# Kernel tuning notes

Measured on AMD Instinct MI355X. Metric: run time of the kernel, lower is better.

The kernel has to match this reference:

```python
import jax, jax.numpy as jnp
import numpy as np
import math

B, T, D = 4, 4096, 1024
H, M = 16, 64
Dh = D // H


def _rope_tables(head_dim, max_seq_len, base=10000):
    inv_freq = 1.0 / (base ** (np.arange(0, head_dim, 2, dtype=np.float32) / head_dim))
    t = np.arange(max_seq_len, dtype=np.float32)
    freqs = np.einsum('i,j->ij', t, inv_freq)  # [T, Dh/2]
    cos = np.cos(freqs)
    sin = np.sin(freqs)
    # interleave (c, c) pairwise -> [T, Dh]
    cos = np.stack((cos, cos), axis=-1).reshape(max_seq_len, head_dim)
    sin = np.stack((sin, sin), axis=-1).reshape(max_seq_len, head_dim)
    return jnp.asarray(cos), jnp.asarray(sin)


def setup_inputs() -> dict:
    key = jax.random.key(0)
    ks = jax.random.split(key, 6)
    s = 1.0 / math.sqrt(D)
    x = jax.random.normal(ks[0], (B, T, D), dtype=jnp.float32)
    Wq = jnp.clip(jax.random.normal(ks[1], (D, D)) * s, -2 * s, 2 * s).astype(jnp.float32)
    Wk = jnp.clip(jax.random.normal(ks[2], (D, D)) * s, -2 * s, 2 * s).astype(jnp.float32)
    Wv = jnp.clip(jax.random.normal(ks[3], (D, D)) * s, -2 * s, 2 * s).astype(jnp.float32)
    Wo = jnp.clip(jax.random.normal(ks[4], (D, D)) * s, -2 * s, 2 * s).astype(jnp.float32)
    latent_code = (jax.random.normal(ks[5], (H, M, Dh)) * 0.02).astype(jnp.float32)
    rope_cos, rope_sin = _rope_tables(Dh, T)
    mask = jnp.ones((B, 1, T, 1), dtype=jnp.int32)
    return {'x': x, 'Wq': Wq, 'Wk': Wk, 'Wv': Wv, 'Wo': Wo,
            'latent_code': latent_code, 'rope_cos': rope_cos,
            'rope_sin': rope_sin, 'mask': mask}


def _rotate(x):
    # (x1, x2) pairs -> (-x2, x1), interleaved
    x2 = x.reshape(*x.shape[:-1], -1, 2)
    return jnp.stack((-x2[..., 1], x2[..., 0]), axis=-1).reshape(x.shape)


def reference(x, Wq, Wk, Wv, Wo, latent_code, rope_cos, rope_sin, mask):
    Bc, Tc, Dc = x.shape
    scale = 1.0 / math.sqrt(Dh)
    # projections -> [B, H, T, Dh]
    q = (x @ Wq.T).reshape(Bc, Tc, H, Dh).transpose(0, 2, 1, 3)
    k = (x @ Wk.T).reshape(Bc, Tc, H, Dh).transpose(0, 2, 1, 3)
    v = (x @ Wv.T).reshape(Bc, Tc, H, Dh).transpose(0, 2, 1, 3)
    cos = rope_cos[:Tc][None, None]  # [1,1,T,Dh]
    sin = rope_sin[:Tc][None, None]
    q = q * cos + _rotate(q) * sin
    k = k * cos + _rotate(k) * sin
    # Stage 1: token -> latent assignment, softmax over tokens (axis=2)
    assign_logits = jnp.einsum('bhtd,hmd->bhtm', k, latent_code) * scale
    assign_logits = jnp.where(mask == 0, -jnp.inf, assign_logits)
    assign = jax.nn.softmax(assign_logits, axis=2)
    k_lat = jnp.einsum('bhtm,bhtd->bhmd', assign, k)
    v_lat = jnp.einsum('bhtm,bhtd->bhmd', assign, v)
    # Stage 2: query attends to latents, softmax over latents (axis=-1)
    att2 = jnp.einsum('bhtd,bhmd->bhtm', q, k_lat) * scale
    p2 = jax.nn.softmax(att2, axis=-1)
    out = jnp.einsum('bhtm,bhmd->bhtd', p2, v_lat)
    out = out.transpose(0, 2, 1, 3).reshape(Bc, Tc, Dc)
    return out @ Wo.T
```

## Files before the change

kernel.cpp:

```cpp
#include <hip/hip_runtime.h>
#include <hip/hip_bf16.h>
#include <stdint.h>


#define DEV static __device__ __forceinline__

using short8 = __attribute__((ext_vector_type(8))) short;
using f32x4  = __attribute__((ext_vector_type(4))) float;

#define ZERO4 (f32x4){0.f, 0.f, 0.f, 0.f}

DEV float bf2f(unsigned short u) {
  union { unsigned int i; float f; } c; c.i = ((unsigned int)u) << 16; return c.f;
}
DEV unsigned short f2bf(float f) {
  __hip_bfloat16 h = __float2bfloat16(f);
  unsigned short u; __builtin_memcpy(&u, &h, 2); return u;
}
DEV f32x4 mfma16(short8 a, short8 b, f32x4 c) {
  return __builtin_amdgcn_mfma_f32_16x16x32_bf16(a, b, c, 0, 0, 0);
}
#define GLOAD_LDS16(G, L) __builtin_amdgcn_global_load_lds( \
    (const __attribute__((address_space(1))) void*)(G),     \
    (__attribute__((address_space(3))) void*)(L), 16, 0, 0)

__global__ void cvt_all(const float* __restrict__ x,
                        const float* __restrict__ Wq, const float* __restrict__ Wk,
                        const float* __restrict__ Wv, const float* __restrict__ Wo,
                        __hip_bfloat16* __restrict__ xb,
                        __hip_bfloat16* __restrict__ Wb) {
  const int bid = blockIdx.x;
  const float* src;
  __hip_bfloat16* dst;
  int base;
  if (bid < 16384) {
    src = x; dst = xb; base = bid;
  } else {
    const int k = (bid - 16384) >> 10;
    src = (k == 0) ? Wq : (k == 1) ? Wk : (k == 2) ? Wv : Wo;
    dst = Wb + (size_t)k * 1048576;
    base = (bid - 16384) & 1023;
  }
  const int i = (base * 256 + threadIdx.x) * 4;
  const float4 v = *(const float4*)(src + i);
  ushort4 o;
  o.x = f2bf(v.x); o.y = f2bf(v.y); o.z = f2bf(v.z); o.w = f2bf(v.w);
  *(ushort4*)(dst + i) = o;
}

template<int MODE, int ROPE>
__global__ __launch_bounds__(256, 4)
void gemm128b(const __hip_bfloat16* __restrict__ A,
              const __hip_bfloat16* __restrict__ Bt,
              void* __restrict__ Cout, __hip_bfloat16* __restrict__ Ct,
              const float* __restrict__ cosT, const float* __restrict__ sinT,
              int M, int N, int K) {
  __shared__ __hip_bfloat16 As[2][128 * 32];
  __shared__ __hip_bfloat16 Bs[2][128 * 32];
  const int tid = threadIdx.x;
  const int w = tid >> 6, l = tid & 63;
  const int lr = l & 15, lg = l >> 4;
  const int rowA0 = blockIdx.x * 128;
  const int colB0 = blockIdx.y * 128;
  const int srow = w * 16 + (l >> 2);
  const int skk  = (l & 3) * 8;
  const __hip_bfloat16* Ab = A  + (size_t)(rowA0 + srow) * K + skk;
  const __hip_bfloat16* Bb = Bt + (size_t)(colB0 + srow) * K + skk;
  f32x4 acc[4][4];
#pragma unroll
  for (int i = 0; i < 4; ++i)
#pragma unroll
    for (int j = 0; j < 4; ++j) acc[i][j] = ZERO4;
  const int wr = (w >> 1) * 64, wc = (w & 1) * 64;
  const int NT = K >> 5;

#define G_STAGE(kt, buf)                                                   \
  {                                                                        \
    const int k0s = (kt) * 32;                                             \
    GLOAD_LDS16(Ab + k0s,                  &As[buf][(w * 16) * 32]);       \
    GLOAD_LDS16(Ab + (size_t)64 * K + k0s, &As[buf][(64 + w * 16) * 32]);  \
    GLOAD_LDS16(Bb + k0s,                  &Bs[buf][(w * 16) * 32]);       \
    GLOAD_LDS16(Bb + (size_t)64 * K + k0s, &Bs[buf][(64 + w * 16) * 32]);  \
  }

  G_STAGE(0, 0);
  for (int kt = 0; kt < NT; ++kt) {
    const int cur = kt & 1;
    if (kt + 1 < NT) {
      G_STAGE(kt + 1, cur ^ 1);
      asm volatile("s_waitcnt vmcnt(4)" ::: "memory");
    } else {
      asm volatile("s_waitcnt vmcnt(0)" ::: "memory");
    }
    __builtin_amdgcn_s_barrier();
    __builtin_amdgcn_s_setprio(1);
    {
      short8 fa[4], fb[4];
#pragma unroll
      for (int i = 0; i < 4; ++i)
        fa[i] = *(const short8*)&As[cur][(wr + i * 16 + lr) * 32 + lg * 8];
#pragma unroll
      for (int j = 0; j < 4; ++j)
        fb[j] = *(const short8*)&Bs[cur][(wc + j * 16 + lr) * 32 + lg * 8];
#pragma unroll
      for (int i = 0; i < 4; ++i)
#pragma unroll
        for (int j = 0; j < 4; ++j)
          acc[i][j] = mfma16(fa[i], fb[j], acc[i][j]);
    }
    __builtin_amdgcn_s_setprio(0);
    __builtin_amdgcn_s_barrier();
  }
#undef G_STAGE

  const int r0 = rowA0 + wr + lg * 4;
  const int c0 = colB0 + wc + lr;
  if (ROPE) {
#pragma unroll
    for (int i = 0; i < 4; ++i)
#pragma unroll
      for (int j = 0; j < 4; ++j)
#pragma unroll
        for (int r = 0; r < 4; ++r) {
          const int m = r0 + i * 16 + r;
          const int n = c0 + j * 16;
          const int t = m & 4095, d = n & 63;
          const float c = cosT[t * 64 + d];
          const float s = sinT[t * 64 + d];
          const float v = acc[i][j][r];
          const float other = __shfl_xor(v, 1, 64);
          acc[i][j][r] = v * c + ((n & 1) ? other : -other) * s;
        }
  }
  if (MODE <= 2) {
#pragma unroll
    for (int i = 0; i < 4; ++i)
#pragma unroll
      for (int j = 0; j < 4; ++j)
#pragma unroll
        for (int r = 0; r < 4; ++r) {
          const size_t idx = (size_t)(r0 + i * 16 + r) * N + (c0 + j * 16);
          if (MODE == 0) ((float*)Cout)[idx] = acc[i][j][r];
          else ((__hip_bfloat16*)Cout)[idx] = __float2bfloat16(acc[i][j][r]);
        }
  }
  if (MODE >= 2) {
#pragma unroll
    for (int i = 0; i < 4; ++i)
#pragma unroll
      for (int j = 0; j < 4; ++j) {
        const int m0 = r0 + i * 16;
        const int n  = c0 + j * 16;
        const size_t row = (size_t)(((m0 >> 12) * 16 + (n >> 6)) * 64 + (n & 63));
        ushort4 pk;
        pk.x = f2bf(acc[i][j][0]); pk.y = f2bf(acc[i][j][1]);
        pk.z = f2bf(acc[i][j][2]); pk.w = f2bf(acc[i][j][3]);
        *(ushort4*)&Ct[row * 4096 + (m0 & 4095)] = pk;
      }
  }
}

__global__ __launch_bounds__(256)
void stage1_expS(const __hip_bfloat16* __restrict__ kmat,
                 const float* __restrict__ latent,
                 const int* __restrict__ mask,
                 __hip_bfloat16* __restrict__ P,
                 float* __restrict__ psum) {
  const int bh = blockIdx.x, chunk = blockIdx.y;
  const int b = bh >> 4, h = bh & 15;
  const int tid = threadIdx.x, w = tid >> 6, l = tid & 63;
  const int lr = l & 15, lg = l >> 4;
  short8 la[4][2];
#pragma unroll
  for (int n = 0; n < 4; ++n)
#pragma unroll
    for (int s = 0; s < 2; ++s) {
      const float* lp = &latent[((size_t)h * 64 + n * 16 + lr) * 64 + s * 32 + lg * 8];
      short8 f;
#pragma unroll
      for (int j = 0; j < 8; ++j) f[j] = (short)f2bf(lp[j]);
      la[n][s] = f;
    }
  float sm[16];
#pragma unroll
  for (int i = 0; i < 16; ++i) sm[i] = 0.f;
  for (int tile = 0; tile < 8; ++tile) {
    const int t = chunk * 512 + tile * 64 + w * 16 + lr;
    const __hip_bfloat16* kp = &kmat[((size_t)(b * 4096 + t) * 16 + h) * 64 + lg * 8];
    const short8 kb0 = *(const short8*)kp;
    const short8 kb1 = *(const short8*)(kp + 32);
    const bool live = (mask[b * 4096 + t] != 0);
    f32x4 acc[4];
#pragma unroll
    for (int n = 0; n < 4; ++n) {
      acc[n] = ZERO4;
      acc[n] = mfma16(la[n][0], kb0, acc[n]);
      acc[n] = mfma16(la[n][1], kb1, acc[n]);
    }
#pragma unroll
    for (int n = 0; n < 4; ++n)
#pragma unroll
      for (int r = 0; r < 4; ++r) {
        const float e = live ? __expf(acc[n][r] * 0.125f) : 0.f;
        const int m = n * 16 + lg * 4 + r;
        ((unsigned short*)P)[((size_t)bh * 64 + m) * 4096 + t] = f2bf(e);
        sm[n * 4 + r] += e;
      }
  }
#pragma unroll
  for (int o = 1; o < 16; o <<= 1)
#pragma unroll
    for (int i = 0; i < 16; ++i) sm[i] += __shfl_xor(sm[i], o, 64);
  if (lr == 0) {
    const size_t pb = ((size_t)(bh * 8 + chunk) * 4 + w) * 64;
#pragma unroll
    for (int n = 0; n < 4; ++n)
#pragma unroll
      for (int r = 0; r < 4; ++r)
        psum[pb + n * 16 + lg * 4 + r] = sm[n * 4 + r];
  }
}

__global__ void denom_inv(const float* __restrict__ psum, float* __restrict__ cinv) {
  const int i = blockIdx.x * 256 + threadIdx.x;
  if (i >= 4096) return;
  const int bh = i >> 6, m = i & 63;
  float sm = 0.f;
#pragma unroll
  for (int c = 0; c < 32; ++c)
    sm += psum[((size_t)bh * 32 + c) * 64 + m];
  cinv[i] = 1.f / sm;
}

__global__ __launch_bounds__(256)
void latgemm7(const __hip_bfloat16* __restrict__ P,
              const __hip_bfloat16* __restrict__ kT,
              const __hip_bfloat16* __restrict__ vT,
              float* __restrict__ partials) {
  const int bh = blockIdx.x;
  const int tid = threadIdx.x, w = tid >> 6, l = tid & 63;
  const int slice = blockIdx.y * 4 + w;
  const int lr = l & 15;
  const int lk = (l >> 4) * 8;
  const size_t base = (size_t)bh * 64 * 4096;
  f32x4 ak[4][4], av[4][4];
#pragma unroll
  for (int i = 0; i < 4; ++i)
#pragma unroll
    for (int j = 0; j < 4; ++j) { ak[i][j] = ZERO4; av[i][j] = ZERO4; }
  for (int ks = 0; ks < 16; ++ks) {
    const int t = slice * 512 + ks * 32 + lk;
    short8 fp[4], fk[4], fv[4];
#pragma unroll
    for (int i = 0; i < 4; ++i) {
      const size_t ro = base + (size_t)(i * 16 + lr) * 4096 + t;
      fp[i] = *(const short8*)&P[ro];
      fk[i] = *(const short8*)&kT[ro];
      fv[i] = *(const short8*)&vT[ro];
    }
#pragma unroll
    for (int i = 0; i < 4; ++i)
#pragma unroll
      for (int j = 0; j < 4; ++j) {
        ak[i][j] = mfma16(fp[i], fk[j], ak[i][j]);
        av[i][j] = mfma16(fv[i], fp[j], av[i][j]);
      }
  }
  float* pk = partials + ((size_t)(slice * 64 + bh)) * 8192;
#pragma unroll
  for (int i = 0; i < 4; ++i)
#pragma unroll
    for (int j = 0; j < 4; ++j)
#pragma unroll
      for (int r = 0; r < 4; ++r) {
        const int row = i * 16 + 4 * (l >> 4) + r;
        const int col = j * 16 + lr;
        pk[(size_t)row * 64 + col]        = ak[i][j][r];
        pk[4096 + (size_t)row * 64 + col] = av[i][j][r];
      }
}

__global__ void latreduce2(const float* __restrict__ partials,
                           const float* __restrict__ cinv,
                           __hip_bfloat16* __restrict__ k_lat,
                           __hip_bfloat16* __restrict__ v_latT) {
  const int i = blockIdx.x * 256 + threadIdx.x;
  const int bh = i >> 13, off = i & 8191;
  float sm = 0.f;
#pragma unroll
  for (int c = 0; c < 8; ++c)
    sm += partials[((size_t)(c * 64 + bh)) * 8192 + off];
  const int m = (off < 4096) ? (off >> 6) : (off & 63);
  sm *= cinv[bh * 64 + m];
  if (off < 4096) k_lat[(size_t)bh * 4096 + off] = __float2bfloat16(sm);
  else            v_latT[(size_t)bh * 4096 + (off - 4096)] = __float2bfloat16(sm);
}

__global__ __launch_bounds__(256)
void stage2_attn(const __hip_bfloat16* __restrict__ q,
                 const __hip_bfloat16* __restrict__ k_lat,
                 const __hip_bfloat16* __restrict__ v_latT,
                 __hip_bfloat16* __restrict__ attn) {
  __shared__ unsigned short Pl[4][16][64];
  const int bid = blockIdx.x;
  const int bh = bid >> 6, tt = (bid & 63) * 64;
  const int b = bh >> 4, h = bh & 15;
  const int tid = threadIdx.x, w = tid >> 6, l = tid & 63;
  const size_t qoff = ((size_t)(b * 4096 + tt + w * 16 + (l & 15)) * 16 + h) * 64;
  const short8 a0 = *(const short8*)&q[qoff + (l >> 4) * 8];
  const short8 a1 = *(const short8*)&q[qoff + 32 + (l >> 4) * 8];
  f32x4 att[4];
#pragma unroll
  for (int n = 0; n < 4; ++n) att[n] = ZERO4;
#pragma unroll
  for (int n = 0; n < 4; ++n) {
    const __hip_bfloat16* kl = &k_lat[((size_t)bh * 64 + n * 16 + (l & 15)) * 64];
    const short8 b0 = *(const short8*)&kl[(l >> 4) * 8];
    const short8 b1 = *(const short8*)&kl[32 + (l >> 4) * 8];
    att[n] = mfma16(a0, b0, att[n]);
    att[n] = mfma16(a1, b1, att[n]);
  }
  float p[4][4];
#pragma unroll
  for (int r = 0; r < 4; ++r) {
    const float v0 = att[0][r] * 0.125f, v1 = att[1][r] * 0.125f;
    const float v2 = att[2][r] * 0.125f, v3 = att[3][r] * 0.125f;
    float mxv = fmaxf(fmaxf(v0, v1), fmaxf(v2, v3));
#pragma unroll
    for (int o = 1; o < 16; o <<= 1) mxv = fmaxf(mxv, __shfl_xor(mxv, o, 64));
    const float e0 = __expf(v0 - mxv), e1 = __expf(v1 - mxv);
    const float e2 = __expf(v2 - mxv), e3 = __expf(v3 - mxv);
    float sum = e0 + e1 + e2 + e3;
#pragma unroll
    for (int o = 1; o < 16; o <<= 1) sum += __shfl_xor(sum, o, 64);
    const float inv = 1.f / sum;
    p[0][r] = e0 * inv; p[1][r] = e1 * inv; p[2][r] = e2 * inv; p[3][r] = e3 * inv;
  }
#pragma unroll
  for (int n = 0; n < 4; ++n)
#pragma unroll
    for (int r = 0; r < 4; ++r) {
      const int row = 4 * (l >> 4) + r;
      const int col = n * 16 + (l & 15);
      Pl[w][row][col ^ ((row & 7) << 3)] = f2bf(p[n][r]);
    }
  __syncthreads();
  const int arow = l & 15;
  const short8 pa0 = *(const short8*)&Pl[w][arow][(((l >> 4) + 0) ^ (arow & 7)) * 8];
  const short8 pa1 = *(const short8*)&Pl[w][arow][(((l >> 4) + 4) ^ (arow & 7)) * 8];
  f32x4 ov[4];
#pragma unroll
  for (int n = 0; n < 4; ++n) ov[n] = ZERO4;
#pragma unroll
  for (int n = 0; n < 4; ++n) {
    const __hip_bfloat16* vt = &v_latT[((size_t)bh * 64 + n * 16 + (l & 15)) * 64];
    const short8 b0 = *(const short8*)&vt[(l >> 4) * 8];
    const short8 b1 = *(const short8*)&vt[32 + (l >> 4) * 8];
    ov[n] = mfma16(pa0, b0, ov[n]);
    ov[n] = mfma16(pa1, b1, ov[n]);
  }
#pragma unroll
  for (int n = 0; n < 4; ++n) {
    const int d = n * 16 + (l & 15);
#pragma unroll
    for (int r = 0; r < 4; ++r) {
      const int trow = tt + w * 16 + 4 * (l >> 4) + r;
      attn[((size_t)(b * 4096 + trow) * 16 + h) * 64 + d] = __float2bfloat16(ov[n][r]);
    }
  }
}

extern "C" void kernel_launch(void* const* d_in, const int* in_sizes, int n_in,
                              void* d_out, int out_size, void* d_ws, size_t ws_size,
                              hipStream_t stream) {
  const float* x      = (const float*)d_in[0];
  const float* Wq     = (const float*)d_in[1];
  const float* Wk     = (const float*)d_in[2];
  const float* Wv     = (const float*)d_in[3];
  const float* Wo     = (const float*)d_in[4];
  const float* latent = (const float*)d_in[5];
  const float* cosT   = (const float*)d_in[6];
  const float* sinT   = (const float*)d_in[7];
  const int*   mask   = (const int*)d_in[8];

  char* ws = (char*)d_ws;
  __hip_bfloat16* xb = (__hip_bfloat16*)ws;
  __hip_bfloat16* Wb = (__hip_bfloat16*)(ws + 33554432);
  __hip_bfloat16* qb = (__hip_bfloat16*)(ws + 41943040);
  __hip_bfloat16* kb = (__hip_bfloat16*)(ws + 75497472);
  __hip_bfloat16* kT = (__hip_bfloat16*)(ws + 109051904);
  __hip_bfloat16* vT = (__hip_bfloat16*)(ws + 142606336);
  char* tail = ws + 176160768;
  float* psum = (float*)tail;
  float* cinv = psum + 131072;
  __hip_bfloat16* k_lat  = (__hip_bfloat16*)(cinv + 4096);
  __hip_bfloat16* v_latT = k_lat + 262144;

  __hip_bfloat16* P    = xb;
  __hip_bfloat16* attn = qb;
  float* partials = (float*)kb;

  cvt_all<<<20480, 256, 0, stream>>>(x, Wq, Wk, Wv, Wo, xb, Wb);

  dim3 gg(128, 8);
  gemm128b<1, 1><<<gg, 256, 0, stream>>>(xb, Wb + 0 * 1048576, qb, nullptr, cosT, sinT, 16384, 1024, 1024);
  gemm128b<2, 1><<<gg, 256, 0, stream>>>(xb, Wb + 1 * 1048576, kb, kT, cosT, sinT, 16384, 1024, 1024);
  gemm128b<3, 0><<<gg, 256, 0, stream>>>(xb, Wb + 2 * 1048576, nullptr, vT, nullptr, nullptr, 16384, 1024, 1024);

  dim3 sg(64, 8);
  stage1_expS<<<sg, 256, 0, stream>>>(kb, latent, mask, P, psum);
  denom_inv<<<16, 256, 0, stream>>>(psum, cinv);

  dim3 lg(64, 2);
  latgemm7<<<lg, 256, 0, stream>>>(P, kT, vT, partials);
  latreduce2<<<2048, 256, 0, stream>>>(partials, cinv, k_lat, v_latT);

  stage2_attn<<<4096, 256, 0, stream>>>(qb, k_lat, v_latT, attn);
  gemm128b<0, 0><<<gg, 256, 0, stream>>>(attn, Wb + 3 * 1048576, d_out, nullptr, nullptr, nullptr, 16384, 1024, 1024);
}
```

Before: 314.0 us.

## Fuse QKV GEMMs into one 256x256-tile swizzled kernel and split latgemm finer

```diff
diff --git a/kernel.cpp b/kernel.cpp
--- a/kernel.cpp
+++ b/kernel.cpp
@@ -48,76 +48,85 @@
   *(ushort4*)(dst + i) = o;
 }
 
-template<int MODE, int ROPE>
-__global__ __launch_bounds__(256, 4)
-void gemm128b(const __hip_bfloat16* __restrict__ A,
+#define GEMM_CORE(A_, B_, K_)                                                     \
+  __shared__ __hip_bfloat16 As[2][256 * 64];                                      \
+  __shared__ __hip_bfloat16 Bs[2][256 * 64];                                      \
+  const int tid = threadIdx.x;                                                    \
+  const int w = tid >> 6, l = tid & 63;                                           \
+  const int lr = l & 15, lg = l >> 4;                                             \
+  const int rowA0 = blockIdx.x * 256;                                             \
+  const int colB0 = blockIdx.y * 256;                                             \
+  const int srow = w * 8 + (l >> 3);                                              \
+  const int skk  = (((l & 7) ^ (l >> 3)) * 8);                                    \
+  const __hip_bfloat16* Ab = A_ + (size_t)(rowA0 + srow) * K_ + skk;              \
+  const __hip_bfloat16* Bb = B_ + (size_t)(colB0 + srow) * K_ + skk;              \
+  f32x4 acc[8][4];                                                                \
+  _Pragma("unroll")                                                               \
+  for (int i = 0; i < 8; ++i)                                                     \
+    _Pragma("unroll")                                                             \
+    for (int j = 0; j < 4; ++j) acc[i][j] = ZERO4;                                \
+  const int wr = (w >> 2) * 128;                                                  \
+  const int wc = (w & 3) * 64;                                                    \
+  const int NT = K_ >> 6;                                                         \
+  {                                                                               \
+    const int k0s = 0;                                                            \
+    _Pragma("unroll")                                                             \
+    for (int i = 0; i < 4; ++i) {                                                 \
+      GLOAD_LDS16(Ab + (size_t)(i * 64) * K_ + k0s, &As[0][i * 4096 + w * 512]);  \
+      GLOAD_LDS16(Bb + (size_t)(i * 64) * K_ + k0s, &Bs[0][i * 4096 + w * 512]);  \
+    }                                                                             \
+  }                                                                               \
+  for (int kt = 0; kt < NT; ++kt) {                                               \
+    const int cur = kt & 1;                                                       \
+    if (kt + 1 < NT) {                                                            \
+      const int k0s = (kt + 1) * 64;                                              \
+      _Pragma("unroll")                                                           \
+      for (int i = 0; i < 4; ++i) {                                               \
+        GLOAD_LDS16(Ab + (size_t)(i * 64) * K_ + k0s, &As[cur ^ 1][i * 4096 + w * 512]); \
+        GLOAD_LDS16(Bb + (size_t)(i * 64) * K_ + k0s, &Bs[cur ^ 1][i * 4096 + w * 512]); \
+      }                                                                           \
+      asm volatile("s_waitcnt vmcnt(8)" ::: "memory");                            \
+    } else {                                                                      \
+      asm volatile("s_waitcnt vmcnt(0)" ::: "memory");                            \
+    }                                                                             \
+    __builtin_amdgcn_s_barrier();                                                 \
+    __builtin_amdgcn_s_setprio(1);                                                \
+    _Pragma("unroll")                                                             \
+    for (int s = 0; s < 2; ++s) {                                                 \
+      short8 fa[8], fb[4];                                                        \
+      _Pragma("unroll")                                                           \
+      for (int i = 0; i < 8; ++i)                                                 \
+        fa[i] = *(const short8*)&As[cur][(wr + i * 16 + lr) * 64 +                \
+                                         (((s * 4 + lg) ^ (lr & 7)) * 8)];        \
+      _Pragma("unroll")                                                           \
+      for (int j = 0; j < 4; ++j)                                                 \
+        fb[j] = *(const short8*)&Bs[cur][(wc + j * 16 + lr) * 64 +                \
+                                         (((s * 4 + lg) ^ (lr & 7)) * 8)];        \
+      _Pragma("unroll")                                                           \
+      for (int i = 0; i < 8; ++i)                                                 \
+        _Pragma("unroll")                                                         \
+        for (int j = 0; j < 4; ++j)                                               \
+          acc[i][j] = mfma16(fa[i], fb[j], acc[i][j]);                            \
+    }                                                                             \
+    __builtin_amdgcn_s_setprio(0);                                                \
+    __builtin_amdgcn_s_barrier();                                                 \
+  }
+
+__global__ __launch_bounds__(512, 2)
+void gemm_qkv(const __hip_bfloat16* __restrict__ A,
               const __hip_bfloat16* __restrict__ Bt,
-              void* __restrict__ Cout, __hip_bfloat16* __restrict__ Ct,
-              const float* __restrict__ cosT, const float* __restrict__ sinT,
-              int M, int N, int K) {
-  __shared__ __hip_bfloat16 As[2][128 * 32];
-  __shared__ __hip_bfloat16 Bs[2][128 * 32];
-  const int tid = threadIdx.x;
-  const int w = tid >> 6, l = tid & 63;
-  const int lr = l & 15, lg = l >> 4;
-  const int rowA0 = blockIdx.x * 128;
-  const int colB0 = blockIdx.y * 128;
-  const int srow = w * 16 + (l >> 2);
-  const int skk  = (l & 3) * 8;
-  const __hip_bfloat16* Ab = A  + (size_t)(rowA0 + srow) * K + skk;
-  const __hip_bfloat16* Bb = Bt + (size_t)(colB0 + srow) * K + skk;
-  f32x4 acc[4][4];
-#pragma unroll
-  for (int i = 0; i < 4; ++i)
-#pragma unroll
-    for (int j = 0; j < 4; ++j) acc[i][j] = ZERO4;
-  const int wr = (w >> 1) * 64, wc = (w & 1) * 64;
-  const int NT = K >> 5;
-
-#define G_STAGE(kt, buf)                                                   \
-  {                                                                        \
-    const int k0s = (kt) * 32;                                             \
-    GLOAD_LDS16(Ab + k0s,                  &As[buf][(w * 16) * 32]);       \
-    GLOAD_LDS16(Ab + (size_t)64 * K + k0s, &As[buf][(64 + w * 16) * 32]);  \
-    GLOAD_LDS16(Bb + k0s,                  &Bs[buf][(w * 16) * 32]);       \
-    GLOAD_LDS16(Bb + (size_t)64 * K + k0s, &Bs[buf][(64 + w * 16) * 32]);  \
-  }
-
-  G_STAGE(0, 0);
-  for (int kt = 0; kt < NT; ++kt) {
-    const int cur = kt & 1;
-    if (kt + 1 < NT) {
-      G_STAGE(kt + 1, cur ^ 1);
-      asm volatile("s_waitcnt vmcnt(4)" ::: "memory");
-    } else {
-      asm volatile("s_waitcnt vmcnt(0)" ::: "memory");
-    }
-    __builtin_amdgcn_s_barrier();
-    __builtin_amdgcn_s_setprio(1);
-    {
-      short8 fa[4], fb[4];
-#pragma unroll
-      for (int i = 0; i < 4; ++i)
-        fa[i] = *(const short8*)&As[cur][(wr + i * 16 + lr) * 32 + lg * 8];
-#pragma unroll
-      for (int j = 0; j < 4; ++j)
-        fb[j] = *(const short8*)&Bs[cur][(wc + j * 16 + lr) * 32 + lg * 8];
-#pragma unroll
-      for (int i = 0; i < 4; ++i)
-#pragma unroll
-        for (int j = 0; j < 4; ++j)
-          acc[i][j] = mfma16(fa[i], fb[j], acc[i][j]);
-    }
-    __builtin_amdgcn_s_setprio(0);
-    __builtin_amdgcn_s_barrier();
-  }
-#undef G_STAGE
-
+              __hip_bfloat16* __restrict__ qb,
+              __hip_bfloat16* __restrict__ kb,
+              __hip_bfloat16* __restrict__ kT,
+              __hip_bfloat16* __restrict__ vT,
+              const float* __restrict__ cosT, const float* __restrict__ sinT) {
+  GEMM_CORE(A, Bt, 1024)
   const int r0 = rowA0 + wr + lg * 4;
   const int c0 = colB0 + wc + lr;
-  if (ROPE) {
-#pragma unroll
-    for (int i = 0; i < 4; ++i)
+  const int panel = blockIdx.y >> 2;
+  if (panel < 2) {
+#pragma unroll
+    for (int i = 0; i < 8; ++i)
 #pragma unroll
       for (int j = 0; j < 4; ++j)
 #pragma unroll
@@ -132,32 +141,49 @@
           acc[i][j][r] = v * c + ((n & 1) ? other : -other) * s;
         }
   }
-  if (MODE <= 2) {
-#pragma unroll
-    for (int i = 0; i < 4; ++i)
+  if (panel < 2) {
+    __hip_bfloat16* Cn = (panel == 0) ? qb : kb;
+#pragma unroll
+    for (int i = 0; i < 8; ++i)
 #pragma unroll
       for (int j = 0; j < 4; ++j)
 #pragma unroll
         for (int r = 0; r < 4; ++r) {
-          const size_t idx = (size_t)(r0 + i * 16 + r) * N + (c0 + j * 16);
-          if (MODE == 0) ((float*)Cout)[idx] = acc[i][j][r];
-          else ((__hip_bfloat16*)Cout)[idx] = __float2bfloat16(acc[i][j][r]);
+          const int nn = (c0 + j * 16) & 1023;
+          Cn[(size_t)(r0 + i * 16 + r) * 1024 + nn] = __float2bfloat16(acc[i][j][r]);
         }
   }
-  if (MODE >= 2) {
-#pragma unroll
-    for (int i = 0; i < 4; ++i)
+  if (panel >= 1) {
+    __hip_bfloat16* Ct = (panel == 1) ? kT : vT;
+#pragma unroll
+    for (int i = 0; i < 8; ++i)
 #pragma unroll
       for (int j = 0; j < 4; ++j) {
         const int m0 = r0 + i * 16;
-        const int n  = c0 + j * 16;
-        const size_t row = (size_t)(((m0 >> 12) * 16 + (n >> 6)) * 64 + (n & 63));
+        const int nn = (c0 + j * 16) & 1023;
+        const size_t row = (size_t)(((m0 >> 12) * 16 + (nn >> 6)) * 64 + (nn & 63));
         ushort4 pk;
         pk.x = f2bf(acc[i][j][0]); pk.y = f2bf(acc[i][j][1]);
         pk.z = f2bf(acc[i][j][2]); pk.w = f2bf(acc[i][j][3]);
         *(ushort4*)&Ct[row * 4096 + (m0 & 4095)] = pk;
       }
   }
+}
+
+__global__ __launch_bounds__(512, 2)
+void gemm_out(const __hip_bfloat16* __restrict__ A,
+              const __hip_bfloat16* __restrict__ Bt,
+              float* __restrict__ Cout) {
+  GEMM_CORE(A, Bt, 1024)
+  const int r0 = rowA0 + wr + lg * 4;
+  const int c0 = colB0 + wc + lr;
+#pragma unroll
+  for (int i = 0; i < 8; ++i)
+#pragma unroll
+    for (int j = 0; j < 4; ++j)
+#pragma unroll
+      for (int r = 0; r < 4; ++r)
+        Cout[(size_t)(r0 + i * 16 + r) * 1024 + (c0 + j * 16)] = acc[i][j][r];
 }
 
 __global__ __launch_bounds__(256)
@@ -248,8 +274,8 @@
   for (int i = 0; i < 4; ++i)
 #pragma unroll
     for (int j = 0; j < 4; ++j) { ak[i][j] = ZERO4; av[i][j] = ZERO4; }
-  for (int ks = 0; ks < 16; ++ks) {
-    const int t = slice * 512 + ks * 32 + lk;
+  for (int ks = 0; ks < 8; ++ks) {
+    const int t = slice * 256 + ks * 32 + lk;
     short8 fp[4], fk[4], fv[4];
 #pragma unroll
     for (int i = 0; i < 4; ++i) {
@@ -288,7 +314,7 @@
   const int bh = i >> 13, off = i & 8191;
   float sm = 0.f;
 #pragma unroll
-  for (int c = 0; c < 8; ++c)
+  for (int c = 0; c < 16; ++c)
     sm += partials[((size_t)(c * 64 + bh)) * 8192 + off];
   const int m = (off < 4096) ? (off >> 6) : (off & 63);
   sm *= cinv[bh * 64 + m];
@@ -395,26 +421,25 @@
   float* cinv = psum + 131072;
   __hip_bfloat16* k_lat  = (__hip_bfloat16*)(cinv + 4096);
   __hip_bfloat16* v_latT = k_lat + 262144;
-
+  float* partials = (float*)kb;
   __hip_bfloat16* P    = xb;
   __hip_bfloat16* attn = qb;
-  float* partials = (float*)kb;
 
   cvt_all<<<20480, 256, 0, stream>>>(x, Wq, Wk, Wv, Wo, xb, Wb);
 
-  dim3 gg(128, 8);
-  gemm128b<1, 1><<<gg, 256, 0, stream>>>(xb, Wb + 0 * 1048576, qb, nullptr, cosT, sinT, 16384, 1024, 1024);
-  gemm128b<2, 1><<<gg, 256, 0, stream>>>(xb, Wb + 1 * 1048576, kb, kT, cosT, sinT, 16384, 1024, 1024);
-  gemm128b<3, 0><<<gg, 256, 0, stream>>>(xb, Wb + 2 * 1048576, nullptr, vT, nullptr, nullptr, 16384, 1024, 1024);
+  dim3 gq(64, 12);
+  gemm_qkv<<<gq, 512, 0, stream>>>(xb, Wb, qb, kb, kT, vT, cosT, sinT);
 
   dim3 sg(64, 8);
   stage1_expS<<<sg, 256, 0, stream>>>(kb, latent, mask, P, psum);
   denom_inv<<<16, 256, 0, stream>>>(psum, cinv);
 
-  dim3 lg(64, 2);
+  dim3 lg(64, 4);
   latgemm7<<<lg, 256, 0, stream>>>(P, kT, vT, partials);
   latreduce2<<<2048, 256, 0, stream>>>(partials, cinv, k_lat, v_latT);
 
   stage2_attn<<<4096, 256, 0, stream>>>(qb, k_lat, v_latT, attn);
-  gemm128b<0, 0><<<gg, 256, 0, stream>>>(attn, Wb + 3 * 1048576, d_out, nullptr, nullptr, nullptr, 16384, 1024, 1024);
-}
+
+  dim3 go(64, 4);
+  gemm_out<<<go, 512, 0, stream>>>(attn, Wb + 3 * 1048576, (float*)d_out);
+}
```

Measured after the change: 294.5 us. 1.07x faster.
